# Optimization experiments

Hardware: AMD Instinct MI355X
Metric: run time of the kernel (lower is better)

## Reference

```python
import jax, jax.numpy as jnp
import numpy as np

L_ORDER = 1
R_ORDER = 1
THRESHOLD = 1.0


def setup_inputs() -> dict:
    key = jax.random.key(0)
    k0, k1, k2, k3, k4 = jax.random.split(key, 5)
    B, T, D, K = 16, 2048, 512, L_ORDER + R_ORDER + 1
    hidden = jax.random.normal(k0, (B, T, D), jnp.float32)
    conv_w = jax.random.normal(k1, (D, 1, K), jnp.float32) / np.sqrt(K).astype(np.float32)
    conv_b = jax.random.normal(k2, (D,), jnp.float32) * 0.05
    lin_w = jax.random.normal(k3, (1, D), jnp.float32) / np.sqrt(D).astype(np.float32)
    lin_b = jax.random.normal(k4, (1,), jnp.float32) * 0.05
    return {"hidden": hidden, "conv_w": conv_w, "conv_b": conv_b, "lin_w": lin_w, "lin_b": lin_b}


def _alphas(hidden, conv_w, conv_b, lin_w, lin_b):
    # hidden: [B, T, D]
    ctx = jnp.transpose(hidden, (0, 2, 1))              # [B, D, T]
    q = jnp.pad(ctx, ((0, 0), (0, 0), (L_ORDER, R_ORDER)))
    mem = jax.lax.conv_general_dilated(
        q, conv_w, (1,), 'VALID',
        dimension_numbers=('NCH', 'OIH', 'NCH'),
        feature_group_count=ctx.shape[1]) + conv_b[None, :, None]   # depthwise conv
    out = jax.nn.relu(jnp.transpose(mem + ctx, (0, 2, 1)))          # [B, T, D] (dropout = identity in eval)
    logits = out @ lin_w.T + lin_b                                  # [B, T, 1]
    return jax.nn.sigmoid(logits)[..., 0]                           # [B, T]


def _cif_scan(hidden, alphas):
    # Sequential integrate-and-fire recurrence over time via lax.scan.
    B, T, H = hidden.shape

    def step(carry, xs):
        integ, frame = carry        # [B], [B, H]
        a, h = xs                   # [B], [B, H]
        dist = 1.0 - integ
        integ = integ + a
        fire_out = integ            # recorded pre-reset (matches torch list_fires)
        fire = integ >= THRESHOLD
        integ = jnp.where(fire, integ - 1.0, integ)
        cur = jnp.where(fire, dist, a)
        rem = a - cur
        frame_out = frame + cur[:, None] * h   # recorded pre-reset
        frame = jnp.where(fire[:, None], rem[:, None] * h, frame_out)
        return (integ, frame), (fire_out, frame_out)

    init = (jnp.zeros((B,), hidden.dtype), jnp.zeros((B, H), hidden.dtype))
    _, (fires, frames) = jax.lax.scan(
        step, init, (alphas.T, jnp.transpose(hidden, (1, 0, 2))))
    return jnp.transpose(fires, (1, 0)), jnp.transpose(frames, (1, 0, 2))  # [B,T], [B,T,H]


def reference(hidden, conv_w, conv_b, lin_w, lin_b):
    B, T, H = hidden.shape
    alphas = _alphas(hidden, conv_w, conv_b, lin_w, lin_b)   # [B, T]
    token_num = alphas.sum(-1)                               # [B]
    fires, frames = _cif_scan(hidden, alphas)
    # Ragged extraction: gather frames at fire positions, left-packed, zero-padded
    # to max_label_len = max(round(sum alphas)). Data-dependent length -> python int.
    max_label_len = int(jnp.max(jnp.round(token_num)))
    fire_mask = fires >= THRESHOLD                           # [B, T]
    rank = jnp.cumsum(fire_mask, axis=1) - 1                 # output slot per fire
    b_idx = jnp.arange(B)[:, None]
    vals = jnp.where(fire_mask[..., None], frames, 0.0)
    acoustic_embeds = jnp.zeros((B, max_label_len, H), hidden.dtype)
    acoustic_embeds = acoustic_embeds.at[b_idx, rank].add(vals, mode='drop')
    return acoustic_embeds, token_num, alphas, fires
```

## Files before the change

### kernel.cpp

```cpp
#include <hip/hip_runtime.h>
#include <math.h>

#define B_ 16
#define T_ 2048
#define D_ 512


__global__ __launch_bounds__(256) void k_alphas(
    const float* __restrict__ hidden,
    const float* __restrict__ conv_w,
    const float* __restrict__ conv_b,
    const float* __restrict__ lin_w,
    const float* __restrict__ lin_b,
    float* __restrict__ alphas_out)
{
    const int b    = blockIdx.y;
    const int wv   = threadIdx.x >> 6;
    const int lane = threadIdx.x & 63;
    const int t0   = blockIdx.x * 64 + wv * 16;
    const int d0   = lane * 8;

    float w0[8], w1[8], w2[8], cb[8], lw[8];
    #pragma unroll
    for (int i = 0; i < 8; ++i) {
        int d = d0 + i;
        w0[i] = conv_w[3 * d];
        w1[i] = conv_w[3 * d + 1];
        w2[i] = conv_w[3 * d + 2];
        cb[i] = conv_b[d];
        lw[i] = lin_w[d];
    }
    const float lb = lin_b[0];

    const float* rbase = hidden + (size_t)b * T_ * D_ + d0;
    auto loadrow = [&](int t, float* f) {
        const float4* p = (const float4*)(rbase + (size_t)t * D_);
        float4 x = p[0], y = p[1];
        f[0]=x.x; f[1]=x.y; f[2]=x.z; f[3]=x.w;
        f[4]=y.x; f[5]=y.y; f[6]=y.z; f[7]=y.w;
    };

    float hm[8], hc[8], hp[8], nx[8];
    if (t0 > 0) { loadrow(t0 - 1, hm); }
    else        { for (int i = 0; i < 8; ++i) hm[i] = 0.f; }
    loadrow(t0, hc);
    loadrow(t0 + 1, hp);

    float* aout = alphas_out + (size_t)b * T_;
    #pragma unroll 4
    for (int j = 0; j < 16; ++j) {
        const int t = t0 + j;
        const int tn = t + 2;
        if (tn < T_) { loadrow(tn, nx); }
        else         { for (int i = 0; i < 8; ++i) nx[i] = 0.f; }

        float dot = 0.f;
        #pragma unroll
        for (int i = 0; i < 8; ++i) {
            float mem = fmaf(hm[i], w0[i],
                        fmaf(hc[i], w1[i],
                        fmaf(hp[i], w2[i], cb[i])));
            float o = mem + hc[i];
            o = o > 0.f ? o : 0.f;
            dot += o * lw[i];
        }
        #pragma unroll
        for (int off = 32; off > 0; off >>= 1) dot += __shfl_down(dot, off);
        if (lane == 0) aout[t] = 1.f / (1.f + expf(-(dot + lb)));

        #pragma unroll
        for (int i = 0; i < 8; ++i) { hm[i] = hc[i]; hc[i] = hp[i]; hp[i] = nx[i]; }
    }
}

__global__ __launch_bounds__(256) void k_scan(
    const float* __restrict__ alphas_in,
    double* __restrict__ S,
    int*    __restrict__ fire_pos,
    int*    __restrict__ n_fires,
    float*  __restrict__ fires_out,
    float*  __restrict__ token_out)
{
    const int b = blockIdx.x, tid = threadIdx.x;
    const size_t base = (size_t)b * T_;

    double a[8], tsum = 0.0;
    #pragma unroll
    for (int i = 0; i < 8; ++i) { a[i] = (double)alphas_in[base + tid * 8 + i]; tsum += a[i]; }

    __shared__ double ssum[256];
    ssum[tid] = tsum;
    __syncthreads();
    for (int off = 1; off < 256; off <<= 1) {
        double v = (tid >= off) ? ssum[tid - off] : 0.0;
        __syncthreads();
        ssum[tid] += v;
        __syncthreads();
    }
    double run = ssum[tid] - tsum;

    #pragma unroll
    for (int i = 0; i < 8; ++i) {
        int t = tid * 8 + i;
        double Sp = run, fp = floor(Sp);
        run += a[i];
        S[base + t] = run;
        fires_out[base + t] = (float)(run - fp);
        if (run >= fp + 1.0) fire_pos[base + (long long)fp] = t;
    }
    if (tid == 255) {
        n_fires[b]   = (int)floor(run);
        token_out[b] = (float)run;
    }
}

__global__ __launch_bounds__(256) void k_gather(
    const float*  __restrict__ hidden,
    const double* __restrict__ S,
    const int*    __restrict__ fire_pos,
    const int*    __restrict__ n_fires,
    float* __restrict__ acoustic, int ML)
{
    const int s = blockIdx.x, b = blockIdx.y;
    float2* dst = (float2*)(acoustic + ((size_t)b * ML + s) * D_) + threadIdx.x;

    int nf = n_fires[b];
    if (nf > ML) nf = ML;
    if (s >= nf) { *dst = make_float2(0.f, 0.f); return; }

    const size_t base = (size_t)b * T_;
    const int t_end   = fire_pos[base + s];
    const int t_start = (s == 0) ? 0 : fire_pos[base + s - 1];

    const double vlo = (double)s, vhi = (double)(s + 1);
    float acc0 = 0.f, acc1 = 0.f;
    double Sp = (t_start == 0) ? 0.0 : S[base + t_start - 1];
    const float* hrow = hidden + (base + (size_t)t_start) * D_ + threadIdx.x * 2;
    for (int t = t_start; t <= t_end; ++t, hrow += D_) {
        double St = S[base + t];
        double wd = fmin(St, vhi) - fmax(Sp, vlo);
        float w = wd > 0.0 ? (float)wd : 0.f;
        float2 hv = *(const float2*)hrow;
        acc0 += w * hv.x;
        acc1 += w * hv.y;
        Sp = St;
    }
    *dst = make_float2(acc0, acc1);
}

extern "C" void kernel_launch(void* const* d_in, const int* in_sizes, int n_in,
                              void* d_out, int out_size, void* d_ws, size_t ws_size,
                              hipStream_t stream) {
    (void)in_sizes; (void)n_in; (void)ws_size;
    const float* hidden = (const float*)d_in[0];
    const float* conv_w = (const float*)d_in[1];
    const float* conv_b = (const float*)d_in[2];
    const float* lin_w  = (const float*)d_in[3];
    const float* lin_b  = (const float*)d_in[4];

    const int B = B_, T = T_, D = D_;
    int ML = (out_size - (B + 2 * B * T)) / (B * D);
    if (ML < 1) ML = 1;

    float* out        = (float*)d_out;
    float* acoustic   = out;
    float* token_out  = out + (size_t)B * ML * D;
    float* alphas_out = token_out + B;
    float* fires_out  = alphas_out + (size_t)B * T;

    double* S        = (double*)d_ws;
    int*    fire_pos = (int*)(S + (size_t)B * T);
    int*    n_fires  = fire_pos + (size_t)B * T;

    k_alphas<<<dim3(T / 64, B), 256, 0, stream>>>(hidden, conv_w, conv_b,
                                                  lin_w, lin_b, alphas_out);
    k_scan<<<B, 256, 0, stream>>>(alphas_out, S, fire_pos, n_fires,
                                  fires_out, token_out);
    k_gather<<<dim3(ML, B), 256, 0, stream>>>(hidden, S, fire_pos, n_fires,
                                              acoustic, ML);
}
```

Measured before the change: 132.0 us.

## Fuse alphas, scan and gather into one cooperative kernel with grid syncs

Merges the three launches into a single cooperative kernel of 512 blocks that uses grid-wide syncs between stages. The prefix scan becomes a per-chunk wave scan plus a cross-chunk reduction over the chunk sums. The gather is a grid-stride loop where each block handles two output rows with float4 loads. This removes two launch gaps and the single-block-per-batch scan, at the cost of grid.sync overhead, an occupancy requirement that every block be co-resident, and a gather spread over fewer threads.

```diff
diff --git a/kernel.cpp b/kernel.cpp
--- a/kernel.cpp
+++ b/kernel.cpp
@@ -1,151 +1,174 @@
 #include <hip/hip_runtime.h>
+#include <hip/hip_cooperative_groups.h>
 #include <math.h>
 
 #define B_ 16
 #define T_ 2048
 #define D_ 512
-
-
-__global__ __launch_bounds__(256) void k_alphas(
+#define NCHUNK_ (T_ / 64)
+
+namespace cg = cooperative_groups;
+
+__global__ __launch_bounds__(256, 2) void k_fused(
     const float* __restrict__ hidden,
     const float* __restrict__ conv_w,
     const float* __restrict__ conv_b,
     const float* __restrict__ lin_w,
     const float* __restrict__ lin_b,
-    float* __restrict__ alphas_out)
+    float*  __restrict__ acoustic,
+    float*  __restrict__ token_out,
+    float*  __restrict__ alphas_out,
+    float*  __restrict__ fires_out,
+    double* __restrict__ S,
+    int*    __restrict__ fire_pos,
+    int*    __restrict__ n_fires,
+    double* __restrict__ chunk_sum,
+    int ML)
 {
+    cg::grid_group grid = cg::this_grid();
+
+    const int c    = blockIdx.x;
     const int b    = blockIdx.y;
     const int wv   = threadIdx.x >> 6;
     const int lane = threadIdx.x & 63;
-    const int t0   = blockIdx.x * 64 + wv * 16;
+    const int t0   = c * 64 + wv * 16;
     const int d0   = lane * 8;
 
-    float w0[8], w1[8], w2[8], cb[8], lw[8];
-    #pragma unroll
-    for (int i = 0; i < 8; ++i) {
-        int d = d0 + i;
-        w0[i] = conv_w[3 * d];
-        w1[i] = conv_w[3 * d + 1];
-        w2[i] = conv_w[3 * d + 2];
-        cb[i] = conv_b[d];
-        lw[i] = lin_w[d];
-    }
-    const float lb = lin_b[0];
-
-    const float* rbase = hidden + (size_t)b * T_ * D_ + d0;
-    auto loadrow = [&](int t, float* f) {
-        const float4* p = (const float4*)(rbase + (size_t)t * D_);
-        float4 x = p[0], y = p[1];
-        f[0]=x.x; f[1]=x.y; f[2]=x.z; f[3]=x.w;
-        f[4]=y.x; f[5]=y.y; f[6]=y.z; f[7]=y.w;
-    };
-
-    float hm[8], hc[8], hp[8], nx[8];
-    if (t0 > 0) { loadrow(t0 - 1, hm); }
-    else        { for (int i = 0; i < 8; ++i) hm[i] = 0.f; }
-    loadrow(t0, hc);
-    loadrow(t0 + 1, hp);
-
-    float* aout = alphas_out + (size_t)b * T_;
-    #pragma unroll 4
-    for (int j = 0; j < 16; ++j) {
-        const int t = t0 + j;
-        const int tn = t + 2;
-        if (tn < T_) { loadrow(tn, nx); }
-        else         { for (int i = 0; i < 8; ++i) nx[i] = 0.f; }
-
-        float dot = 0.f;
+    __shared__ float salpha[64];
+
+    {
+        float w0[8], w1[8], w2[8], cb[8], lw[8];
         #pragma unroll
         for (int i = 0; i < 8; ++i) {
-            float mem = fmaf(hm[i], w0[i],
-                        fmaf(hc[i], w1[i],
-                        fmaf(hp[i], w2[i], cb[i])));
-            float o = mem + hc[i];
-            o = o > 0.f ? o : 0.f;
-            dot += o * lw[i];
-        }
+            int d = d0 + i;
+            w0[i] = conv_w[3 * d];
+            w1[i] = conv_w[3 * d + 1];
+            w2[i] = conv_w[3 * d + 2];
+            cb[i] = conv_b[d];
+            lw[i] = lin_w[d];
+        }
+        const float lb = lin_b[0];
+
+        const float* rbase = hidden + (size_t)b * T_ * D_ + d0;
+        auto loadrow = [&](int t, float* f) {
+            const float4* p = (const float4*)(rbase + (size_t)t * D_);
+            float4 x = p[0], y = p[1];
+            f[0]=x.x; f[1]=x.y; f[2]=x.z; f[3]=x.w;
+            f[4]=y.x; f[5]=y.y; f[6]=y.z; f[7]=y.w;
+        };
+
+        float hm[8], hc[8], hp[8], nx[8];
+        if (t0 > 0) { loadrow(t0 - 1, hm); }
+        else        { for (int i = 0; i < 8; ++i) hm[i] = 0.f; }
+        loadrow(t0, hc);
+        loadrow(t0 + 1, hp);
+
+        float* aout = alphas_out + (size_t)b * T_;
+        #pragma unroll 4
+        for (int j = 0; j < 16; ++j) {
+            const int t = t0 + j;
+            const int tn = t + 2;
+            if (tn < T_) { loadrow(tn, nx); }
+            else         { for (int i = 0; i < 8; ++i) nx[i] = 0.f; }
+
+            float dot = 0.f;
+            #pragma unroll
+            for (int i = 0; i < 8; ++i) {
+                float mem = fmaf(hm[i], w0[i],
+                            fmaf(hc[i], w1[i],
+                            fmaf(hp[i], w2[i], cb[i])));
+                float o = mem + hc[i];
+                o = o > 0.f ? o : 0.f;
+                dot += o * lw[i];
+            }
+            #pragma unroll
+            for (int off = 32; off > 0; off >>= 1) dot += __shfl_down(dot, off);
+            if (lane == 0) {
+                float av = 1.f / (1.f + expf(-(dot + lb)));
+                aout[t] = av;
+                salpha[wv * 16 + j] = av;
+            }
+            #pragma unroll
+            for (int i = 0; i < 8; ++i) { hm[i] = hc[i]; hc[i] = hp[i]; hp[i] = nx[i]; }
+        }
+    }
+    __syncthreads();
+
+    double a_j = 0.0, incl = 0.0;
+    if (wv == 0) {
+        a_j  = (double)salpha[lane];
+        incl = a_j;
         #pragma unroll
-        for (int off = 32; off > 0; off >>= 1) dot += __shfl_down(dot, off);
-        if (lane == 0) aout[t] = 1.f / (1.f + expf(-(dot + lb)));
-
+        for (int off = 1; off < 64; off <<= 1) {
+            double v = __shfl_up(incl, off);
+            if (lane >= off) incl += v;
+        }
+        if (lane == 63) chunk_sum[b * NCHUNK_ + c] = incl;
+    }
+
+    grid.sync();
+
+    if (wv == 0) {
+        double v = (lane < c) ? chunk_sum[b * NCHUNK_ + lane] : 0.0;
         #pragma unroll
-        for (int i = 0; i < 8; ++i) { hm[i] = hc[i]; hc[i] = hp[i]; hp[i] = nx[i]; }
-    }
-}
-
-__global__ __launch_bounds__(256) void k_scan(
-    const float* __restrict__ alphas_in,
-    double* __restrict__ S,
-    int*    __restrict__ fire_pos,
-    int*    __restrict__ n_fires,
-    float*  __restrict__ fires_out,
-    float*  __restrict__ token_out)
-{
-    const int b = blockIdx.x, tid = threadIdx.x;
-    const size_t base = (size_t)b * T_;
-
-    double a[8], tsum = 0.0;
-    #pragma unroll
-    for (int i = 0; i < 8; ++i) { a[i] = (double)alphas_in[base + tid * 8 + i]; tsum += a[i]; }
-
-    __shared__ double ssum[256];
-    ssum[tid] = tsum;
-    __syncthreads();
-    for (int off = 1; off < 256; off <<= 1) {
-        double v = (tid >= off) ? ssum[tid - off] : 0.0;
-        __syncthreads();
-        ssum[tid] += v;
-        __syncthreads();
-    }
-    double run = ssum[tid] - tsum;
-
-    #pragma unroll
-    for (int i = 0; i < 8; ++i) {
-        int t = tid * 8 + i;
-        double Sp = run, fp = floor(Sp);
-        run += a[i];
-        S[base + t] = run;
-        fires_out[base + t] = (float)(run - fp);
-        if (run >= fp + 1.0) fire_pos[base + (long long)fp] = t;
-    }
-    if (tid == 255) {
-        n_fires[b]   = (int)floor(run);
-        token_out[b] = (float)run;
-    }
-}
-
-__global__ __launch_bounds__(256) void k_gather(
-    const float*  __restrict__ hidden,
-    const double* __restrict__ S,
-    const int*    __restrict__ fire_pos,
-    const int*    __restrict__ n_fires,
-    float* __restrict__ acoustic, int ML)
-{
-    const int s = blockIdx.x, b = blockIdx.y;
-    float2* dst = (float2*)(acoustic + ((size_t)b * ML + s) * D_) + threadIdx.x;
-
-    int nf = n_fires[b];
-    if (nf > ML) nf = ML;
-    if (s >= nf) { *dst = make_float2(0.f, 0.f); return; }
-
-    const size_t base = (size_t)b * T_;
-    const int t_end   = fire_pos[base + s];
-    const int t_start = (s == 0) ? 0 : fire_pos[base + s - 1];
-
-    const double vlo = (double)s, vhi = (double)(s + 1);
-    float acc0 = 0.f, acc1 = 0.f;
-    double Sp = (t_start == 0) ? 0.0 : S[base + t_start - 1];
-    const float* hrow = hidden + (base + (size_t)t_start) * D_ + threadIdx.x * 2;
-    for (int t = t_start; t <= t_end; ++t, hrow += D_) {
-        double St = S[base + t];
-        double wd = fmin(St, vhi) - fmax(Sp, vlo);
-        float w = wd > 0.0 ? (float)wd : 0.f;
-        float2 hv = *(const float2*)hrow;
-        acc0 += w * hv.x;
-        acc1 += w * hv.y;
-        Sp = St;
-    }
-    *dst = make_float2(acc0, acc1);
+        for (int off = 32; off > 0; off >>= 1) v += __shfl_down(v, off);
+        const double base = __shfl(v, 0);
+
+        const int t     = c * 64 + lane;
+        const size_t bt = (size_t)b * T_ + t;
+        const double run  = base + incl;
+        const double excl = run - a_j;
+        const double fp   = floor(excl);
+        S[bt] = run;
+        fires_out[bt] = (float)(run - fp);
+        if (run >= fp + 1.0)
+            fire_pos[(size_t)b * T_ + (long long)fp] = t;
+        if (c == NCHUNK_ - 1 && lane == 63) {
+            n_fires[b]   = (int)floor(run);
+            token_out[b] = (float)run;
+        }
+    }
+
+    grid.sync();
+
+    {
+        const int nblk  = NCHUNK_ * B_;
+        const int flat  = b * NCHUNK_ + c;
+        const int total = ML * B_;
+        const int half  = threadIdx.x >> 7;
+        const int tq    = threadIdx.x & 127;
+
+        for (int u0 = flat * 2; u0 < total; u0 += nblk * 2) {
+            const int u = u0 + half;
+            if (u >= total) continue;
+            const int gb = u / ML;
+            const int s  = u - gb * ML;
+
+            float4* dst = (float4*)(acoustic + ((size_t)gb * ML + s) * D_) + tq;
+            int nf = n_fires[gb];
+            if (nf > ML) nf = ML;
+            if (s >= nf) { *dst = make_float4(0.f, 0.f, 0.f, 0.f); continue; }
+
+            const size_t gbase = (size_t)gb * T_;
+            const int t_end    = fire_pos[gbase + s];
+            const int t_start  = (s == 0) ? 0 : fire_pos[gbase + s - 1];
+
+            const double vlo = (double)s, vhi = (double)(s + 1);
+            float a0 = 0.f, a1 = 0.f, a2 = 0.f, a3 = 0.f;
+            double Sp = (t_start == 0) ? 0.0 : S[gbase + t_start - 1];
+            const float4* hrow =
+                (const float4*)(hidden + (gbase + (size_t)t_start) * D_) + tq;
+            for (int t = t_start; t <= t_end; ++t, hrow += D_ / 4) {
+                double St = S[gbase + t];
+                double wd = fmin(St, vhi) - fmax(Sp, vlo);
+                float w = wd > 0.0 ? (float)wd : 0.f;
+                float4 hv = *hrow;
+                a0 += w * hv.x; a1 += w * hv.y; a2 += w * hv.z; a3 += w * hv.w;
+                Sp = St;
+            }
+            *dst = make_float4(a0, a1, a2, a3);
+        }
+    }
 }
 
 extern "C" void kernel_launch(void* const* d_in, const int* in_sizes, int n_in,
@@ -168,14 +191,16 @@
     float* alphas_out = token_out + B;
     float* fires_out  = alphas_out + (size_t)B * T;
 
-    double* S        = (double*)d_ws;
-    int*    fire_pos = (int*)(S + (size_t)B * T);
-    int*    n_fires  = fire_pos + (size_t)B * T;
-
-    k_alphas<<<dim3(T / 64, B), 256, 0, stream>>>(hidden, conv_w, conv_b,
-                                                  lin_w, lin_b, alphas_out);
-    k_scan<<<B, 256, 0, stream>>>(alphas_out, S, fire_pos, n_fires,
-                                  fires_out, token_out);
-    k_gather<<<dim3(ML, B), 256, 0, stream>>>(hidden, S, fire_pos, n_fires,
-                                              acoustic, ML);
+    double* S         = (double*)d_ws;
+    int*    fire_pos  = (int*)(S + (size_t)B * T);
+    int*    n_fires   = fire_pos + (size_t)B * T;
+    double* chunk_sum = (double*)(n_fires + B);
+
+    void* kargs[] = {
+        (void*)&hidden, (void*)&conv_w, (void*)&conv_b, (void*)&lin_w, (void*)&lin_b,
+        (void*)&acoustic, (void*)&token_out, (void*)&alphas_out, (void*)&fires_out,
+        (void*)&S, (void*)&fire_pos, (void*)&n_fires, (void*)&chunk_sum, (void*)&ML
+    };
+    hipLaunchCooperativeKernel((const void*)k_fused, dim3(NCHUNK_, B),
+                               dim3(256), kargs, 0, stream);
 }
```

New measurement: 259.9 us. 96.9% more time.
